# Kernel tuning notes

Hardware: AMD Instinct MI355X
Metric: run time of the kernel (lower is better)

The kernel has to match this reference:

```python
import jax, jax.numpy as jnp
import numpy as np

N_NODES = 100000
N_EDGES = 1600000
NFEAT, NHID, NCLASS = 128, 64, 40
DROPOUT_P = 0.5


def setup_inputs() -> dict:
    key = jax.random.key(0)
    k1, k2, k3, k4 = jax.random.split(key, 4)
    inputs = jax.random.normal(k1, (N_NODES, NFEAT), dtype=jnp.float32)
    edge_index = jax.random.randint(k2, (2, N_EDGES), 0, N_NODES, dtype=jnp.int64)
    # Glorot-uniform-ish init like torch Linear / PyG GCNConv
    lim1 = float(np.sqrt(6.0 / (NFEAT + NHID)))
    lim2 = float(np.sqrt(6.0 / (NHID + NCLASS)))
    W1 = jax.random.uniform(k3, (NFEAT, NHID), minval=-lim1, maxval=lim1, dtype=jnp.float32)
    W2 = jax.random.uniform(k4, (NHID, NCLASS), minval=-lim2, maxval=lim2, dtype=jnp.float32)
    b1 = jnp.zeros((NHID,), dtype=jnp.float32)
    b2 = jnp.zeros((NCLASS,), dtype=jnp.float32)
    return {"inputs": inputs, "edge_index": edge_index, "W1": W1, "b1": b1, "W2": W2, "b2": b2}


def _gcn_conv(x, W, b, src, dst, norm, n_nodes):
    # PyG GCNConv: out[i] = sum_{j->i} norm_ij * (x W)[j] + b
    xw = x @ W                              # [N, out_dim]
    msg = xw[src] * norm[:, None]           # [E+N, out_dim] gather + scale
    out = jax.ops.segment_sum(msg, dst, num_segments=n_nodes)  # scatter-add
    return out + b


def reference(inputs, edge_index, W1, b1, W2, b2):
    n = inputs.shape[0]
    loops = jnp.arange(n, dtype=edge_index.dtype)
    src = jnp.concatenate([edge_index[0], loops])   # add self-loops
    dst = jnp.concatenate([edge_index[1], loops])
    # symmetric normalization D^{-1/2} (A+I) D^{-1/2}
    deg = jax.ops.segment_sum(jnp.ones_like(src, dtype=inputs.dtype), dst, num_segments=n)
    dis = jnp.where(deg > 0, jax.lax.rsqrt(jnp.maximum(deg, 1.0)), 0.0)
    norm = dis[src] * dis[dst]
    # dropout on inputs (training mode, fixed key for determinism)
    keep = jax.random.bernoulli(jax.random.key(42), 1.0 - DROPOUT_P, inputs.shape)
    x = jnp.where(keep, inputs / (1.0 - DROPOUT_P), 0.0)
    h = jax.nn.relu(_gcn_conv(x, W1, b1, src, dst, norm, n))
    out = _gcn_conv(h, W2, b2, src, dst, norm, n)
    return out
```

## Files before the change

kernel.cpp:

```cpp
#include <hip/hip_runtime.h>

#define NF 128
#define NH 64
#define NC 40
#define BSHIFT 10
#define NB 98
#define BIN_T 8192
#define BSTRIDE 20480

typedef __attribute__((ext_vector_type(8))) short short8;
typedef __attribute__((ext_vector_type(4))) float float4v;

__device__ __forceinline__ unsigned rotl32(unsigned v, int s) { return (v << s) | (v >> (32 - s)); }

__device__ __forceinline__ unsigned short f2bf(float f) {
  unsigned u = __float_as_uint(f);
  return (unsigned short)((u + 0x7FFFu + ((u >> 16) & 1u)) >> 16);
}
__device__ __forceinline__ float bf2f(unsigned short b) {
  return __uint_as_float(((unsigned)b) << 16);
}

__device__ __forceinline__ unsigned threefry_bits(unsigned idx) {
  const unsigned k0 = 0u, k1 = 42u;
  const unsigned k2x = 0u ^ 42u ^ 0x1BD11BDAu;
  unsigned x0 = 0u, x1 = idx;
  x0 += k0; x1 += k1;
  x0 += x1; x1 = rotl32(x1, 13); x1 ^= x0;
  x0 += x1; x1 = rotl32(x1, 15); x1 ^= x0;
  x0 += x1; x1 = rotl32(x1, 26); x1 ^= x0;
  x0 += x1; x1 = rotl32(x1, 6);  x1 ^= x0;
  x0 += k1; x1 += k2x + 1u;
  x0 += x1; x1 = rotl32(x1, 17); x1 ^= x0;
  x0 += x1; x1 = rotl32(x1, 29); x1 ^= x0;
  x0 += x1; x1 = rotl32(x1, 16); x1 ^= x0;
  x0 += x1; x1 = rotl32(x1, 24); x1 ^= x0;
  x0 += k2x; x1 += k0 + 2u;
  x0 += x1; x1 = rotl32(x1, 13); x1 ^= x0;
  x0 += x1; x1 = rotl32(x1, 15); x1 ^= x0;
  x0 += x1; x1 = rotl32(x1, 26); x1 ^= x0;
  x0 += x1; x1 = rotl32(x1, 6);  x1 ^= x0;
  x0 += k0; x1 += k1 + 3u;
  x0 += x1; x1 = rotl32(x1, 17); x1 ^= x0;
  x0 += x1; x1 = rotl32(x1, 29); x1 ^= x0;
  x0 += x1; x1 = rotl32(x1, 16); x1 ^= x0;
  x0 += x1; x1 = rotl32(x1, 24); x1 ^= x0;
  x0 += k1; x1 += k2x + 4u;
  x0 += x1; x1 = rotl32(x1, 13); x1 ^= x0;
  x0 += x1; x1 = rotl32(x1, 15); x1 ^= x0;
  x0 += x1; x1 = rotl32(x1, 26); x1 ^= x0;
  x0 += x1; x1 = rotl32(x1, 6);  x1 ^= x0;
  x0 += k2x; x1 += k0 + 5u;
  return x0 ^ x1;
}

__global__ __launch_bounds__(256) void k_bin(const int* __restrict__ src, const int* __restrict__ dst,
                                             int* __restrict__ gcur, unsigned* __restrict__ binned,
                                             const float* __restrict__ W1, const float* __restrict__ W2,
                                             unsigned short* __restrict__ Wt1b, unsigned short* __restrict__ Wt2b,
                                             int nE, int nbin) {
  int t = threadIdx.x;
  if (blockIdx.x >= nbin) {
    int id = (blockIdx.x - nbin) * 256 + t;
    if (id < NF * NH) {
      int k = id >> 6, c = id & 63;
      Wt1b[c * NF + k] = f2bf(W1[id]);
    } else if (id < NF * NH + 48 * NH) {
      int id2 = id - NF * NH;
      int c = id2 >> 6, k = id2 & 63;
      Wt2b[c * NH + k] = (c < NC) ? f2bf(W2[k * NC + c]) : 0;
    }
    return;
  }
  __shared__ int h[NB];
  __shared__ int off[NB];
  int b0 = blockIdx.x * BIN_T;
  int b1 = b0 + BIN_T; if (b1 > nE) b1 = nE;
  if (t < NB) h[t] = 0;
  __syncthreads();
  for (int e = b0 + t; e < b1; e += 256)
    atomicAdd(&h[dst[e] >> BSHIFT], 1);
  __syncthreads();
  if (t < NB && h[t] > 0) off[t] = t * BSTRIDE + atomicAdd(&gcur[t], h[t]);
  __syncthreads();
  for (int e = b0 + t; e < b1; e += 256) {
    int s = src[e], d = dst[e];
    int p = atomicAdd(&off[d >> BSHIFT], 1);
    binned[p] = ((unsigned)s << BSHIFT) | (unsigned)(d & ((1 << BSHIFT) - 1));
  }
}

__global__ __launch_bounds__(1024) void k_fillb(const unsigned* __restrict__ binned, const int* __restrict__ gcur,
                                                unsigned* __restrict__ rpd, float* __restrict__ dis,
                                                int* __restrict__ csrc, int n) {
  __shared__ int hist[1024];
  __shared__ int sbuf[1024];
  int b = blockIdx.x;
  int base = b << BSHIFT;
  int t = threadIdx.x;
  int lo = b * BSTRIDE, hi = lo + gcur[b];
  hist[t] = 0;
  __syncthreads();
  for (int e = lo + t; e < hi; e += 1024)
    atomicAdd(&hist[binned[e] & 1023u], 1);
  __syncthreads();
  int v = hist[t];
  sbuf[t] = v; __syncthreads();
  for (int off = 1; off < 1024; off <<= 1) {
    int u = (t >= off) ? sbuf[t - off] : 0; __syncthreads();
    sbuf[t] += u; __syncthreads();
  }
  int excl = sbuf[t] - v;
  if (base + t < n) {
    rpd[base + t] = ((unsigned)(lo + excl) << 11) | (unsigned)v;
    dis[base + t] = rsqrtf((float)(v + 1));
  }
  __syncthreads();
  hist[t] = lo + excl;
  __syncthreads();
  for (int e = lo + t; e < hi; e += 1024) {
    unsigned p = binned[e];
    int pos = atomicAdd(&hist[p & 1023u], 1);
    csrc[pos] = (int)(p >> BSHIFT);
  }
}

__global__ __launch_bounds__(256) void k_xw(const float* __restrict__ x, const unsigned short* __restrict__ Wt1b,
                                            const float* __restrict__ dis, unsigned short* __restrict__ y1b, int n) {
  __shared__ unsigned short Ws[NH * 136];
  __shared__ unsigned short xs[16 * 136];
  int t = threadIdx.x;
  int nodeBase = blockIdx.x * 16;
  for (int id = t; id < NH * 16; id += 256) {
    int c = id >> 4, kc = id & 15;
    *(short8*)&Ws[c * 136 + kc * 8] = *(const short8*)&Wt1b[c * NF + kc * 8];
  }
  {
    int nloc = t >> 4, kbase = (t & 15) * 8;
    int ebase = (nodeBase + nloc) * NF + kbase;
    const float4* xp = (const float4*)x;
    float4 a = xp[(ebase >> 2)];
    float4 b = xp[(ebase >> 2) + 1];
    float v[8] = {a.x, a.y, a.z, a.w, b.x, b.y, b.z, b.w};
#pragma unroll
    for (int q = 0; q < 8; ++q) {
      unsigned idx = (unsigned)(ebase + q);
      bool keep = (threefry_bits(idx) & 0x80000000u) == 0u;
      xs[nloc * 136 + kbase + q] = keep ? f2bf(v[q] * 2.0f) : 0;
    }
  }
  __syncthreads();
  int w = t >> 6, lane = t & 63;
  int m = lane & 15, quad = lane >> 4;
  float4v acc = {0.f, 0.f, 0.f, 0.f};
#pragma unroll
  for (int ks = 0; ks < 4; ++ks) {
    short8 a = *(const short8*)&xs[m * 136 + ks * 32 + quad * 8];
    short8 b = *(const short8*)&Ws[(w * 16 + m) * 136 + ks * 32 + quad * 8];
    acc = __builtin_amdgcn_mfma_f32_16x16x32_bf16(a, b, acc, 0, 0, 0);
  }
#pragma unroll
  for (int r = 0; r < 4; ++r) {
    int node = nodeBase + quad * 4 + r;
    y1b[node * NH + w * 16 + m] = f2bf(acc[r] * dis[node]);
  }
}

#define ACC8(u) \
  a0 += __uint_as_float((u).x << 16); \
  a1 += __uint_as_float((u).x & 0xFFFF0000u); \
  a2 += __uint_as_float((u).y << 16); \
  a3 += __uint_as_float((u).y & 0xFFFF0000u); \
  a4 += __uint_as_float((u).z << 16); \
  a5 += __uint_as_float((u).z & 0xFFFF0000u); \
  a6 += __uint_as_float((u).w << 16); \
  a7 += __uint_as_float((u).w & 0xFFFF0000u);

__device__ __forceinline__ unsigned packbf(float lo, float hi) {
  return (unsigned)f2bf(lo) | ((unsigned)f2bf(hi) << 16);
}

__global__ __launch_bounds__(256) void k_agg1(const unsigned short* __restrict__ y1b, const unsigned* __restrict__ rpd,
                                              const int* __restrict__ csrc, const float* __restrict__ dis,
                                              const float* __restrict__ b1, unsigned short* __restrict__ gb, int n) {
  int i = blockIdx.x * 32 + (threadIdx.x >> 3);
  if (i >= n) return;
  int fl = (threadIdx.x & 7) << 3;
  const uint4 us = *(const uint4*)&y1b[(i << 6) + fl];
  float a0 = __uint_as_float(us.x << 16);
  float a1 = __uint_as_float(us.x & 0xFFFF0000u);
  float a2 = __uint_as_float(us.y << 16);
  float a3 = __uint_as_float(us.y & 0xFFFF0000u);
  float a4 = __uint_as_float(us.z << 16);
  float a5 = __uint_as_float(us.z & 0xFFFF0000u);
  float a6 = __uint_as_float(us.w << 16);
  float a7 = __uint_as_float(us.w & 0xFFFF0000u);
  unsigned rd = rpd[i];
  int lo = (int)(rd >> 11), hi = lo + (int)(rd & 2047u);
  int e = lo;
  int s0, s1, s2, s3;
  if (e + 4 <= hi) { s0 = csrc[e]; s1 = csrc[e + 1]; s2 = csrc[e + 2]; s3 = csrc[e + 3]; }
  for (; e + 8 <= hi; e += 4) {
    uint4 u0 = *(const uint4*)&y1b[(s0 << 6) + fl];
    uint4 u1 = *(const uint4*)&y1b[(s1 << 6) + fl];
    uint4 u2 = *(const uint4*)&y1b[(s2 << 6) + fl];
    uint4 u3 = *(const uint4*)&y1b[(s3 << 6) + fl];
    s0 = csrc[e + 4]; s1 = csrc[e + 5]; s2 = csrc[e + 6]; s3 = csrc[e + 7];
    ACC8(u0) ACC8(u1) ACC8(u2) ACC8(u3)
  }
  if (e + 4 <= hi) {
    uint4 u0 = *(const uint4*)&y1b[(s0 << 6) + fl];
    uint4 u1 = *(const uint4*)&y1b[(s1 << 6) + fl];
    uint4 u2 = *(const uint4*)&y1b[(s2 << 6) + fl];
    uint4 u3 = *(const uint4*)&y1b[(s3 << 6) + fl];
    ACC8(u0) ACC8(u1) ACC8(u2) ACC8(u3)
    e += 4;
  }
  for (; e < hi; ++e) {
    int s = csrc[e];
    uint4 u = *(const uint4*)&y1b[(s << 6) + fl];
    ACC8(u)
  }
  float di = dis[i];
  float4 bb0 = *(const float4*)&b1[fl];
  float4 bb1 = *(const float4*)&b1[fl + 4];
  uint4 o;
  o.x = packbf(di * fmaxf(fmaf(di, a0, bb0.x), 0.f), di * fmaxf(fmaf(di, a1, bb0.y), 0.f));
  o.y = packbf(di * fmaxf(fmaf(di, a2, bb0.z), 0.f), di * fmaxf(fmaf(di, a3, bb0.w), 0.f));
  o.z = packbf(di * fmaxf(fmaf(di, a4, bb1.x), 0.f), di * fmaxf(fmaf(di, a5, bb1.y), 0.f));
  o.w = packbf(di * fmaxf(fmaf(di, a6, bb1.z), 0.f), di * fmaxf(fmaf(di, a7, bb1.w), 0.f));
  *(uint4*)&gb[(i << 6) + fl] = o;
}

__global__ __launch_bounds__(256) void k_aggg(const unsigned short* __restrict__ gb, const unsigned* __restrict__ rpd,
                                              const int* __restrict__ csrc, const float* __restrict__ dis,
                                              unsigned short* __restrict__ ahb, int n) {
  int i = blockIdx.x * 32 + (threadIdx.x >> 3);
  if (i >= n) return;
  int fl = (threadIdx.x & 7) << 3;
  const uint4 us = *(const uint4*)&gb[(i << 6) + fl];
  float a0 = __uint_as_float(us.x << 16);
  float a1 = __uint_as_float(us.x & 0xFFFF0000u);
  float a2 = __uint_as_float(us.y << 16);
  float a3 = __uint_as_float(us.y & 0xFFFF0000u);
  float a4 = __uint_as_float(us.z << 16);
  float a5 = __uint_as_float(us.z & 0xFFFF0000u);
  float a6 = __uint_as_float(us.w << 16);
  float a7 = __uint_as_float(us.w & 0xFFFF0000u);
  unsigned rd = rpd[i];
  int lo = (int)(rd >> 11), hi = lo + (int)(rd & 2047u);
  int e = lo;
  int s0, s1, s2, s3;
  if (e + 4 <= hi) { s0 = csrc[e]; s1 = csrc[e + 1]; s2 = csrc[e + 2]; s3 = csrc[e + 3]; }
  for (; e + 8 <= hi; e += 4) {
    uint4 u0 = *(const uint4*)&gb[(s0 << 6) + fl];
    uint4 u1 = *(const uint4*)&gb[(s1 << 6) + fl];
    uint4 u2 = *(const uint4*)&gb[(s2 << 6) + fl];
    uint4 u3 = *(const uint4*)&gb[(s3 << 6) + fl];
    s0 = csrc[e + 4]; s1 = csrc[e + 5]; s2 = csrc[e + 6]; s3 = csrc[e + 7];
    ACC8(u0) ACC8(u1) ACC8(u2) ACC8(u3)
  }
  if (e + 4 <= hi) {
    uint4 u0 = *(const uint4*)&gb[(s0 << 6) + fl];
    uint4 u1 = *(const uint4*)&gb[(s1 << 6) + fl];
    uint4 u2 = *(const uint4*)&gb[(s2 << 6) + fl];
    uint4 u3 = *(const uint4*)&gb[(s3 << 6) + fl];
    ACC8(u0) ACC8(u1) ACC8(u2) ACC8(u3)
    e += 4;
  }
  for (; e < hi; ++e) {
    int s = csrc[e];
    uint4 u = *(const uint4*)&gb[(s << 6) + fl];
    ACC8(u)
  }
  float di = dis[i];
  uint4 o;
  o.x = packbf(di * a0, di * a1);
  o.y = packbf(di * a2, di * a3);
  o.z = packbf(di * a4, di * a5);
  o.w = packbf(di * a6, di * a7);
  *(uint4*)&ahb[(i << 6) + fl] = o;
}

__global__ __launch_bounds__(192) void k_hw2(const unsigned short* __restrict__ ahb, const unsigned short* __restrict__ Wt2b,
                                             const float* __restrict__ b2, float* __restrict__ out, int n) {
  __shared__ unsigned short Ws[48 * 72];
  __shared__ unsigned short xs[16 * 72];
  int t = threadIdx.x;
  int nodeBase = blockIdx.x * 16;
  for (int id = t; id < 48 * 8; id += 192) {
    int c = id >> 3, kc = id & 7;
    *(short8*)&Ws[c * 72 + kc * 8] = *(const short8*)&Wt2b[c * NH + kc * 8];
  }
  if (t < 128) {
    int c = t >> 3, kc = t & 7;
    *(short8*)&xs[c * 72 + kc * 8] = *(const short8*)&ahb[(nodeBase + c) * NH + kc * 8];
  }
  __syncthreads();
  int w = t >> 6, lane = t & 63;
  int m = lane & 15, quad = lane >> 4;
  float4v acc = {0.f, 0.f, 0.f, 0.f};
#pragma unroll
  for (int ks = 0; ks < 2; ++ks) {
    short8 a = *(const short8*)&xs[m * 72 + ks * 32 + quad * 8];
    short8 b = *(const short8*)&Ws[(w * 16 + m) * 72 + ks * 32 + quad * 8];
    acc = __builtin_amdgcn_mfma_f32_16x16x32_bf16(a, b, acc, 0, 0, 0);
  }
  int col = w * 16 + m;
  if (col < NC) {
    float bias = b2[col];
#pragma unroll
    for (int r = 0; r < 4; ++r) {
      int node = nodeBase + quad * 4 + r;
      out[node * NC + col] = acc[r] + bias;
    }
  }
}

extern "C" void kernel_launch(void* const* d_in, const int* in_sizes, int n_in,
                              void* d_out, int out_size, void* d_ws, size_t ws_size,
                              hipStream_t stream) {
  const float* x  = (const float*)d_in[0];
  const int*   ei = (const int*)d_in[1];
  const float* W1 = (const float*)d_in[2];
  const float* b1 = (const float*)d_in[3];
  const float* W2 = (const float*)d_in[4];
  const float* b2 = (const float*)d_in[5];
  float* out = (float*)d_out;
  int n  = in_sizes[0] / NF;
  int nE = in_sizes[1] / 2;
  const int* src = ei;
  const int* dst = ei + nE;

  char* ws = (char*)d_ws;
  float*    dis  = (float*)(ws + 0);
  unsigned* rpd  = (unsigned*)(ws + 400000);
  int*      gcur = (int*)(ws + 800000);
  unsigned short* Wt1b = (unsigned short*)(ws + 800512);
  unsigned short* Wt2b = (unsigned short*)(ws + 816896);
  int*      csrc = (int*)(ws + 823296);
  unsigned short* y1b = (unsigned short*)(ws + 8851456);
  unsigned short* gb  = (unsigned short*)(ws + 21651456);
  unsigned* binned = (unsigned*)(ws + 21651456);
  unsigned short* ahb = y1b;

  hipMemsetAsync(gcur, 0, NB * 4, stream);

  int nbin = (nE + BIN_T - 1) / BIN_T;
  int nprep = (NF * NH + 48 * NH + 255) / 256;
  k_bin  <<<nbin + nprep, 256, 0, stream>>>(src, dst, gcur, binned, W1, W2, Wt1b, Wt2b, nE, nbin);
  k_fillb<<<NB, 1024, 0, stream>>>(binned, gcur, rpd, dis, csrc, n);
  k_xw   <<<n / 16, 256, 0, stream>>>(x, Wt1b, dis, y1b, n);
  k_agg1 <<<(n + 31) / 32, 256, 0, stream>>>(y1b, rpd, csrc, dis, b1, gb, n);
  k_aggg <<<(n + 31) / 32, 256, 0, stream>>>(gb, rpd, csrc, dis, ahb, n);
  k_hw2  <<<n / 16, 192, 0, stream>>>(ahb, Wt2b, b2, out, n);
}
```

Measured before the change: 230.2 us.

## Fuse layer-2 aggregation with W2 matmul and use wave-shuffle scan

Merges the second aggregation kernel with the hidden-by-W2 MFMA kernel. The aggregated rows now go straight into shared memory, so the intermediate bf16 buffer is never written to or read back from global memory and one launch is removed. The block-wide prefix scan in the CSR fill kernel is replaced with wavefront shuffle scans plus a small cross-wave scan, which cuts the number of barriers. The dis and bias loads in agg1 are also hoisted ahead of the gather loop. In exchange, a wave of the fused kernel sits idle during the MFMA phase and W2 is reloaded into shared memory by every block.

```diff
diff --git a/kernel.cpp b/kernel.cpp
--- a/kernel.cpp
+++ b/kernel.cpp
@@ -94,7 +94,7 @@
                                                 unsigned* __restrict__ rpd, float* __restrict__ dis,
                                                 int* __restrict__ csrc, int n) {
   __shared__ int hist[1024];
-  __shared__ int sbuf[1024];
+  __shared__ int wsum[16];
   int b = blockIdx.x;
   int base = b << BSHIFT;
   int t = threadIdx.x;
@@ -105,12 +105,27 @@
     atomicAdd(&hist[binned[e] & 1023u], 1);
   __syncthreads();
   int v = hist[t];
-  sbuf[t] = v; __syncthreads();
-  for (int off = 1; off < 1024; off <<= 1) {
-    int u = (t >= off) ? sbuf[t - off] : 0; __syncthreads();
-    sbuf[t] += u; __syncthreads();
-  }
-  int excl = sbuf[t] - v;
+  int sv = v;
+#pragma unroll
+  for (int off = 1; off < 64; off <<= 1) {
+    int u = __shfl_up(sv, off);
+    if ((t & 63) >= off) sv += u;
+  }
+  int wid = t >> 6;
+  if ((t & 63) == 63) wsum[wid] = sv;
+  __syncthreads();
+  if (t < 16) {
+    int ws = wsum[t];
+    int sws = ws;
+#pragma unroll
+    for (int off = 1; off < 16; off <<= 1) {
+      int u = __shfl_up(sws, off);
+      if (t >= off) sws += u;
+    }
+    wsum[t] = sws - ws;
+  }
+  __syncthreads();
+  int excl = sv - v + wsum[wid];
   if (base + t < n) {
     rpd[base + t] = ((unsigned)(lo + excl) << 11) | (unsigned)v;
     dis[base + t] = rsqrtf((float)(v + 1));
@@ -186,6 +201,9 @@
   int i = blockIdx.x * 32 + (threadIdx.x >> 3);
   if (i >= n) return;
   int fl = (threadIdx.x & 7) << 3;
+  float di = dis[i];
+  float4 bb0 = *(const float4*)&b1[fl];
+  float4 bb1 = *(const float4*)&b1[fl + 4];
   const uint4 us = *(const uint4*)&y1b[(i << 6) + fl];
   float a0 = __uint_as_float(us.x << 16);
   float a1 = __uint_as_float(us.x & 0xFFFF0000u);
@@ -221,9 +239,6 @@
     uint4 u = *(const uint4*)&y1b[(s << 6) + fl];
     ACC8(u)
   }
-  float di = dis[i];
-  float4 bb0 = *(const float4*)&b1[fl];
-  float4 bb1 = *(const float4*)&b1[fl + 4];
   uint4 o;
   o.x = packbf(di * fmaxf(fmaf(di, a0, bb0.x), 0.f), di * fmaxf(fmaf(di, a1, bb0.y), 0.f));
   o.y = packbf(di * fmaxf(fmaf(di, a2, bb0.z), 0.f), di * fmaxf(fmaf(di, a3, bb0.w), 0.f));
@@ -232,87 +247,86 @@
   *(uint4*)&gb[(i << 6) + fl] = o;
 }
 
-__global__ __launch_bounds__(256) void k_aggg(const unsigned short* __restrict__ gb, const unsigned* __restrict__ rpd,
+__global__ __launch_bounds__(256) void k_agg2(const unsigned short* __restrict__ gb, const unsigned* __restrict__ rpd,
                                               const int* __restrict__ csrc, const float* __restrict__ dis,
-                                              unsigned short* __restrict__ ahb, int n) {
-  int i = blockIdx.x * 32 + (threadIdx.x >> 3);
-  if (i >= n) return;
-  int fl = (threadIdx.x & 7) << 3;
-  const uint4 us = *(const uint4*)&gb[(i << 6) + fl];
-  float a0 = __uint_as_float(us.x << 16);
-  float a1 = __uint_as_float(us.x & 0xFFFF0000u);
-  float a2 = __uint_as_float(us.y << 16);
-  float a3 = __uint_as_float(us.y & 0xFFFF0000u);
-  float a4 = __uint_as_float(us.z << 16);
-  float a5 = __uint_as_float(us.z & 0xFFFF0000u);
-  float a6 = __uint_as_float(us.w << 16);
-  float a7 = __uint_as_float(us.w & 0xFFFF0000u);
-  unsigned rd = rpd[i];
-  int lo = (int)(rd >> 11), hi = lo + (int)(rd & 2047u);
-  int e = lo;
-  int s0, s1, s2, s3;
-  if (e + 4 <= hi) { s0 = csrc[e]; s1 = csrc[e + 1]; s2 = csrc[e + 2]; s3 = csrc[e + 3]; }
-  for (; e + 8 <= hi; e += 4) {
-    uint4 u0 = *(const uint4*)&gb[(s0 << 6) + fl];
-    uint4 u1 = *(const uint4*)&gb[(s1 << 6) + fl];
-    uint4 u2 = *(const uint4*)&gb[(s2 << 6) + fl];
-    uint4 u3 = *(const uint4*)&gb[(s3 << 6) + fl];
-    s0 = csrc[e + 4]; s1 = csrc[e + 5]; s2 = csrc[e + 6]; s3 = csrc[e + 7];
-    ACC8(u0) ACC8(u1) ACC8(u2) ACC8(u3)
-  }
-  if (e + 4 <= hi) {
-    uint4 u0 = *(const uint4*)&gb[(s0 << 6) + fl];
-    uint4 u1 = *(const uint4*)&gb[(s1 << 6) + fl];
-    uint4 u2 = *(const uint4*)&gb[(s2 << 6) + fl];
-    uint4 u3 = *(const uint4*)&gb[(s3 << 6) + fl];
-    ACC8(u0) ACC8(u1) ACC8(u2) ACC8(u3)
-    e += 4;
-  }
-  for (; e < hi; ++e) {
-    int s = csrc[e];
-    uint4 u = *(const uint4*)&gb[(s << 6) + fl];
-    ACC8(u)
-  }
-  float di = dis[i];
-  uint4 o;
-  o.x = packbf(di * a0, di * a1);
-  o.y = packbf(di * a2, di * a3);
-  o.z = packbf(di * a4, di * a5);
-  o.w = packbf(di * a6, di * a7);
-  *(uint4*)&ahb[(i << 6) + fl] = o;
-}
-
-__global__ __launch_bounds__(192) void k_hw2(const unsigned short* __restrict__ ahb, const unsigned short* __restrict__ Wt2b,
-                                             const float* __restrict__ b2, float* __restrict__ out, int n) {
+                                              const unsigned short* __restrict__ Wt2b, const float* __restrict__ b2,
+                                              float* __restrict__ out, int n) {
   __shared__ unsigned short Ws[48 * 72];
-  __shared__ unsigned short xs[16 * 72];
+  __shared__ unsigned short ahs[32 * 72];
   int t = threadIdx.x;
-  int nodeBase = blockIdx.x * 16;
-  for (int id = t; id < 48 * 8; id += 192) {
+  int nodeBase = blockIdx.x * 32;
+  for (int id = t; id < 48 * 8; id += 256) {
     int c = id >> 3, kc = id & 7;
     *(short8*)&Ws[c * 72 + kc * 8] = *(const short8*)&Wt2b[c * NH + kc * 8];
   }
-  if (t < 128) {
-    int c = t >> 3, kc = t & 7;
-    *(short8*)&xs[c * 72 + kc * 8] = *(const short8*)&ahb[(nodeBase + c) * NH + kc * 8];
+  int i = nodeBase + (t >> 3);
+  int fl = (t & 7) << 3;
+  if (i < n) {
+    float di = dis[i];
+    const uint4 us = *(const uint4*)&gb[(i << 6) + fl];
+    float a0 = __uint_as_float(us.x << 16);
+    float a1 = __uint_as_float(us.x & 0xFFFF0000u);
+    float a2 = __uint_as_float(us.y << 16);
+    float a3 = __uint_as_float(us.y & 0xFFFF0000u);
+    float a4 = __uint_as_float(us.z << 16);
+    float a5 = __uint_as_float(us.z & 0xFFFF0000u);
+    float a6 = __uint_as_float(us.w << 16);
+    float a7 = __uint_as_float(us.w & 0xFFFF0000u);
+    unsigned rd = rpd[i];
+    int lo = (int)(rd >> 11), hi = lo + (int)(rd & 2047u);
+    int e = lo;
+    int s0, s1, s2, s3;
+    if (e + 4 <= hi) { s0 = csrc[e]; s1 = csrc[e + 1]; s2 = csrc[e + 2]; s3 = csrc[e + 3]; }
+    for (; e + 8 <= hi; e += 4) {
+      uint4 u0 = *(const uint4*)&gb[(s0 << 6) + fl];
+      uint4 u1 = *(const uint4*)&gb[(s1 << 6) + fl];
+      uint4 u2 = *(const uint4*)&gb[(s2 << 6) + fl];
+      uint4 u3 = *(const uint4*)&gb[(s3 << 6) + fl];
+      s0 = csrc[e + 4]; s1 = csrc[e + 5]; s2 = csrc[e + 6]; s3 = csrc[e + 7];
+      ACC8(u0) ACC8(u1) ACC8(u2) ACC8(u3)
+    }
+    if (e + 4 <= hi) {
+      uint4 u0 = *(const uint4*)&gb[(s0 << 6) + fl];
+      uint4 u1 = *(const uint4*)&gb[(s1 << 6) + fl];
+      uint4 u2 = *(const uint4*)&gb[(s2 << 6) + fl];
+      uint4 u3 = *(const uint4*)&gb[(s3 << 6) + fl];
+      ACC8(u0) ACC8(u1) ACC8(u2) ACC8(u3)
+      e += 4;
+    }
+    for (; e < hi; ++e) {
+      int s = csrc[e];
+      uint4 u = *(const uint4*)&gb[(s << 6) + fl];
+      ACC8(u)
+    }
+    uint4 o;
+    o.x = packbf(di * a0, di * a1);
+    o.y = packbf(di * a2, di * a3);
+    o.z = packbf(di * a4, di * a5);
+    o.w = packbf(di * a6, di * a7);
+    *(uint4*)&ahs[(t >> 3) * 72 + fl] = o;
   }
   __syncthreads();
   int w = t >> 6, lane = t & 63;
   int m = lane & 15, quad = lane >> 4;
-  float4v acc = {0.f, 0.f, 0.f, 0.f};
-#pragma unroll
-  for (int ks = 0; ks < 2; ++ks) {
-    short8 a = *(const short8*)&xs[m * 72 + ks * 32 + quad * 8];
-    short8 b = *(const short8*)&Ws[(w * 16 + m) * 72 + ks * 32 + quad * 8];
-    acc = __builtin_amdgcn_mfma_f32_16x16x32_bf16(a, b, acc, 0, 0, 0);
-  }
-  int col = w * 16 + m;
-  if (col < NC) {
-    float bias = b2[col];
-#pragma unroll
-    for (int r = 0; r < 4; ++r) {
-      int node = nodeBase + quad * 4 + r;
-      out[node * NC + col] = acc[r] + bias;
+  if (w < 3) {
+#pragma unroll
+    for (int mt = 0; mt < 2; ++mt) {
+      float4v acc = {0.f, 0.f, 0.f, 0.f};
+#pragma unroll
+      for (int ks = 0; ks < 2; ++ks) {
+        short8 a = *(const short8*)&ahs[(mt * 16 + m) * 72 + ks * 32 + quad * 8];
+        short8 b = *(const short8*)&Ws[(w * 16 + m) * 72 + ks * 32 + quad * 8];
+        acc = __builtin_amdgcn_mfma_f32_16x16x32_bf16(a, b, acc, 0, 0, 0);
+      }
+      int col = w * 16 + m;
+      if (col < NC) {
+        float bias = b2[col];
+#pragma unroll
+        for (int r = 0; r < 4; ++r) {
+          int node = nodeBase + mt * 16 + quad * 4 + r;
+          if (node < n) out[node * NC + col] = acc[r] + bias;
+        }
+      }
     }
   }
 }
@@ -342,7 +356,6 @@
   unsigned short* y1b = (unsigned short*)(ws + 8851456);
   unsigned short* gb  = (unsigned short*)(ws + 21651456);
   unsigned* binned = (unsigned*)(ws + 21651456);
-  unsigned short* ahb = y1b;
 
   hipMemsetAsync(gcur, 0, NB * 4, stream);
 
@@ -352,6 +365,5 @@
   k_fillb<<<NB, 1024, 0, stream>>>(binned, gcur, rpd, dis, csrc, n);
   k_xw   <<<n / 16, 256, 0, stream>>>(x, Wt1b, dis, y1b, n);
   k_agg1 <<<(n + 31) / 32, 256, 0, stream>>>(y1b, rpd, csrc, dis, b1, gb, n);
-  k_aggg <<<(n + 31) / 32, 256, 0, stream>>>(gb, rpd, csrc, dis, ahb, n);
-  k_hw2  <<<n / 16, 192, 0, stream>>>(ahb, Wt2b, b2, out, n);
-}
+  k_agg2 <<<(n + 31) / 32, 256, 0, stream>>>(gb, rpd, csrc, dis, Wt2b, b2, out, n);
+}
```

New measurement: 223.6 us. 2.9% less time.
